# Optimization experiments

Hardware: AMD Instinct MI355X
Metric: run time of the kernel (lower is better)

## Reference

```python
import jax, jax.numpy as jnp
import numpy as np

T, B, E, H = 128, 1024, 1024, 1024  # batch must equal hidden (original code uses Whh @ h)


def setup_inputs() -> dict:
    key = jax.random.key(0)
    ks = jax.random.split(key, 10)
    s = 1.0 / np.sqrt(H).astype(np.float32)  # ~xavier scale, avoids gate saturation
    inp = {
        'X': jax.random.normal(ks[0], (T, B, E), dtype=jnp.float32),
        'Wii': jax.random.normal(ks[1], (E, H), dtype=jnp.float32) * s,
        'Whi': jax.random.normal(ks[2], (H, H), dtype=jnp.float32) * s,
        'bi': jnp.zeros((H,), dtype=jnp.float32),
        'Wif': jax.random.normal(ks[3], (E, H), dtype=jnp.float32) * s,
        'Whf': jax.random.normal(ks[4], (H, H), dtype=jnp.float32) * s,
        'bf': jnp.zeros((H,), dtype=jnp.float32),
        'Wig': jax.random.normal(ks[5], (E, H), dtype=jnp.float32) * s,
        'Whg': jax.random.normal(ks[6], (H, H), dtype=jnp.float32) * s,
        'bg': jnp.zeros((H,), dtype=jnp.float32),
        'Wio': jax.random.normal(ks[7], (E, H), dtype=jnp.float32) * s,
        'Who': jax.random.normal(ks[8], (H, H), dtype=jnp.float32) * s,
        'bo': jnp.zeros((H,), dtype=jnp.float32),
    }
    return inp


def reference(X, Wii, Whi, bi, Wif, Whf, bf, Wig, Whg, bg, Wio, Who, bo):
    # Faithful to the original: recurrent term is Whh @ h (NOT h @ Whh),
    # which requires batch == hidden as in the source module.
    batch = X.shape[1]
    hid = Wii.shape[1]
    h0 = jnp.zeros((batch, hid), dtype=X.dtype)
    c0 = jnp.zeros((batch, hid), dtype=X.dtype)

    def step(carry, x_t):
        h, c = carry
        i = jax.nn.sigmoid(x_t @ Wii + Whi @ h + bi)
        f = jax.nn.sigmoid(x_t @ Wif + Whf @ h + bf)
        g = jnp.tanh(x_t @ Wig + Whg @ h + bg)
        o = jax.nn.sigmoid(x_t @ Wio + Who @ h + bo)
        c_new = f * c + i * g
        h_new = o * jnp.tanh(c_new)
        return (h_new, c_new), h_new

    (h_t, c_t), hidden_sequence = jax.lax.scan(step, (h0, c0), X)
    return hidden_sequence, (h_t, c_t)
```

## Files before the change

kernel.cpp:

```cpp
#include <hip/hip_runtime.h>
#include <cstdint>

typedef __attribute__((ext_vector_type(8))) short bf16x8;
typedef __attribute__((ext_vector_type(4))) float f32x4;

#define AS1 __attribute__((address_space(1)))
#define AS3 __attribute__((address_space(3)))

__device__ __forceinline__ unsigned short f2bf(float f) {
  unsigned int u = __builtin_bit_cast(unsigned int, f);
  return (unsigned short)((u + 0x7fffu + ((u >> 16) & 1u)) >> 16);
}
__device__ __forceinline__ float bf2f(unsigned short h) {
  unsigned int u = ((unsigned int)h) << 16;
  return __builtin_bit_cast(float, u);
}
__device__ __forceinline__ float sigm(float x) { return 1.f / (1.f + __expf(-x)); }
__device__ __forceinline__ float tanh_f(float x) {
  float e = __expf(2.f * x);
  return 1.f - 2.f / (e + 1.f);
}
__device__ __forceinline__ void gload16(const void* g, void* l) {
  __builtin_amdgcn_global_load_lds((const AS1 unsigned int*)g, (AS3 unsigned int*)l, 16, 0, 0);
}
__device__ __forceinline__ int swz(int e) { return e ^ (((e >> 6) & 7) << 3); }


__global__ __launch_bounds__(256) void conv_wh_kernel(
    const float4* __restrict__ w0, const float4* __restrict__ w1,
    const float4* __restrict__ w2, const float4* __restrict__ w3,
    unsigned long long* __restrict__ dst) {
  int i = blockIdx.x * 256 + threadIdx.x;
  int g = i >> 18;
  const float4* s = g == 0 ? w0 : g == 1 ? w1 : g == 2 ? w2 : w3;
  float4 v = s[i & 0x3FFFF];
  unsigned long long p = (unsigned long long)f2bf(v.x) |
                         ((unsigned long long)f2bf(v.y) << 16) |
                         ((unsigned long long)f2bf(v.z) << 32) |
                         ((unsigned long long)f2bf(v.w) << 48);
  dst[i] = p;
}

__global__ __launch_bounds__(256) void conv_wiT_kernel(
    const float* __restrict__ w0, const float* __restrict__ w1,
    const float* __restrict__ w2, const float* __restrict__ w3,
    unsigned short* __restrict__ dst) {
  __shared__ unsigned short ls[64][72];
  int bid = blockIdx.x;
  int g = bid >> 8;
  int t2 = bid & 255;
  int tj = t2 & 15, tk = t2 >> 4;
  const float* W = g == 0 ? w0 : g == 1 ? w1 : g == 2 ? w2 : w3;
  int k0 = tk * 64, j0 = tj * 64;
  int ty = threadIdx.x >> 6, tx = threadIdx.x & 63;
#pragma unroll
  for (int r = 0; r < 16; ++r) {
    int k = k0 + ty * 16 + r;
    ls[tx][ty * 16 + r] = f2bf(W[k * 1024 + j0 + tx]);
  }
  __syncthreads();
#pragma unroll
  for (int r = 0; r < 16; ++r) {
    int jl = ty * 16 + r;
    dst[(size_t)(g * 1024 + j0 + jl) * 1024 + k0 + tx] = ls[jl][tx];
  }
}

__global__ __launch_bounds__(256) void conv_bias_kernel(
    const float* __restrict__ b0, const float* __restrict__ b1,
    const float* __restrict__ b2, const float* __restrict__ b3,
    float* __restrict__ dst) {
  int i = blockIdx.x * 256 + threadIdx.x;
  const float* s = (i >> 10) == 0 ? b0 : (i >> 10) == 1 ? b1 : (i >> 10) == 2 ? b2 : b3;
  dst[i] = s[i & 1023];
}

__global__ __launch_bounds__(256) void conv_x_kernel(
    const float4* __restrict__ src, unsigned long long* __restrict__ dst, int n4) {
  int i = blockIdx.x * 256 + threadIdx.x;
  if (i < n4) {
    float4 v = src[i];
    dst[i] = (unsigned long long)f2bf(v.x) |
             ((unsigned long long)f2bf(v.y) << 16) |
             ((unsigned long long)f2bf(v.z) << 32) |
             ((unsigned long long)f2bf(v.w) << 48);
  }
}

__global__ __launch_bounds__(256, 3) void xproj_gemm_kernel(
    const unsigned short* __restrict__ A,
    const unsigned short* __restrict__ Bt,
    unsigned short* __restrict__ C,
    int Mc) {
  __shared__ __align__(16) char smem[34816];
  unsigned short* lsA = (unsigned short*)smem;
  unsigned short* lsB = lsA + 8192;
  int xcd = blockIdx.x & 7;
  int i5 = blockIdx.x >> 3;
  int bn = xcd * 4 + (i5 & 3);
  int bm = i5 >> 2;
  int m0 = bm * 128, n0 = bn * 128;
  int tid = threadIdx.x, w = tid >> 6, lane = tid & 63;
  int wm = w >> 1, wn = w & 1;
  int l15 = lane & 15, l4 = lane >> 4;

  f32x4 acc[4][4];
#pragma unroll
  for (int i = 0; i < 4; ++i)
#pragma unroll
    for (int j = 0; j < 4; ++j) acc[i][j] = (f32x4)0.f;

  for (int ks = 0; ks < 16; ++ks) {
    int kk = ks * 64;
    __syncthreads();
#pragma unroll
    for (int ld = 0; ld < 4; ++ld) {
      int cid = ld * 256 + tid;
      int r = cid >> 3, kc = (cid & 7) * 8;
      int sk = kk + (kc ^ ((r & 7) << 3));
      gload16(&A[(size_t)(m0 + r) * 1024 + sk], &lsA[(ld * 256 + w * 64) * 8]);
      gload16(&Bt[(size_t)(n0 + r) * 1024 + sk], &lsB[(ld * 256 + w * 64) * 8]);
    }
    __syncthreads();
    bf16x8 af[4][2], bfr[4][2];
#pragma unroll
    for (int cm = 0; cm < 4; ++cm)
#pragma unroll
      for (int kss = 0; kss < 2; ++kss) {
        int e = (wm * 64 + cm * 16 + l15) * 64 + kss * 32 + l4 * 8;
        af[cm][kss] = *(const bf16x8*)&lsA[swz(e)];
      }
#pragma unroll
    for (int cn = 0; cn < 4; ++cn)
#pragma unroll
      for (int kss = 0; kss < 2; ++kss) {
        int e = (wn * 64 + cn * 16 + l15) * 64 + kss * 32 + l4 * 8;
        bfr[cn][kss] = *(const bf16x8*)&lsB[swz(e)];
      }
    __builtin_amdgcn_s_setprio(1);
#pragma unroll
    for (int cm = 0; cm < 4; ++cm)
#pragma unroll
      for (int cn = 0; cn < 4; ++cn)
#pragma unroll
        for (int kss = 0; kss < 2; ++kss)
          acc[cm][cn] = __builtin_amdgcn_mfma_f32_16x16x32_bf16(
              af[cm][kss], bfr[cn][kss], acc[cm][cn], 0, 0, 0);
    __builtin_amdgcn_s_setprio(0);
  }

  __syncthreads();
  unsigned short* lsC = (unsigned short*)smem;
#pragma unroll
  for (int cm = 0; cm < 4; ++cm)
#pragma unroll
    for (int cn = 0; cn < 4; ++cn)
#pragma unroll
      for (int r = 0; r < 4; ++r) {
        int row = wm * 64 + cm * 16 + l4 * 4 + r;
        int col = wn * 64 + cn * 16 + l15;
        lsC[row * 136 + col] = f2bf(acc[cm][cn][r]);
      }
  __syncthreads();
#pragma unroll
  for (int u = 0; u < 8; ++u) {
    int chunk = u * 256 + tid;
    int row = chunk >> 4, c8 = chunk & 15;
    bf16x8 v = *(const bf16x8*)&lsC[row * 136 + c8 * 8];
    *(bf16x8*)&C[(size_t)(m0 + row) * 4096 + n0 + c8 * 8] = v;
  }
}

__global__ __launch_bounds__(256) void lstm_step_kernel(
    const unsigned short* __restrict__ Wh,
    const unsigned short* __restrict__ hT,
    const unsigned short* __restrict__ Xp,
    const float* __restrict__ bias,
    float* __restrict__ cst,
    float* __restrict__ out_h,
    float* __restrict__ out_ht,
    float* __restrict__ out_ct,
    unsigned short* __restrict__ hT_next,
    int isLast) {
  __shared__ unsigned short lsA[3][128 * 64];
  __shared__ unsigned short lsB[3][64 * 64];
  int bx = blockIdx.x;
  int xcd = bx & 7, idx = bx >> 3;
  int bb = xcd * 4 + (idx & 3);
  int bj = idx >> 2;
  int b0 = bb * 32, j0 = bj * 64;
  int tid = threadIdx.x, w = tid >> 6, lane = tid & 63;
  int wm = w >> 1, wn = w & 1;
  int l15 = lane & 15, l4 = lane >> 4;
  int bbase = b0 + wm * 16 + l4 * 4;

  float bias_pre[4][2];
  float c_pre[2][4];
  unsigned short xp_pre[4][2][4];
#pragma unroll
  for (int n = 0; n < 2; ++n) {
    int j = j0 + wn * 32 + n * 16 + l15;
#pragma unroll
    for (int g = 0; g < 4; ++g) bias_pre[g][n] = bias[g * 1024 + j];
#pragma unroll
    for (int r = 0; r < 4; ++r) {
      c_pre[n][r] = cst[(size_t)(bbase + r) * 1024 + j];
#pragma unroll
      for (int g = 0; g < 4; ++g)
        xp_pre[g][n][r] = Xp[(size_t)(bbase + r) * 4096 + g * 1024 + j];
    }
  }

  f32x4 acc[4][2];
#pragma unroll
  for (int g = 0; g < 4; ++g)
#pragma unroll
    for (int n = 0; n < 2; ++n) acc[g][n] = (f32x4)0.f;

  auto stage = [&](int buf, int kk) {
#pragma unroll
    for (int ld = 0; ld < 4; ++ld) {
      int cid = ld * 256 + tid;
      int r = cid >> 3, kc = (cid & 7) * 8;
      int sk = kk + (kc ^ ((r & 7) << 3));
      int grow = ((r >> 4) & 3) * 1024 + b0 + (r >> 6) * 16 + (r & 15);
      gload16(&Wh[(size_t)grow * 1024 + sk], &lsA[buf][(ld * 256 + w * 64) * 8]);
    }
#pragma unroll
    for (int u = 0; u < 2; ++u) {
      int cid = u * 256 + tid;
      int r = cid >> 3, kc = (cid & 7) * 8;
      int sk = kk + (kc ^ ((r & 7) << 3));
      gload16(&hT[(size_t)(j0 + r) * 1024 + sk], &lsB[buf][(u * 256 + w * 64) * 8]);
    }
  };
  auto compute = [&](int buf) {
    bf16x8 af[4][2], bfr[2][2];
#pragma unroll
    for (int g = 0; g < 4; ++g)
#pragma unroll
      for (int kss = 0; kss < 2; ++kss) {
        int e = (wm * 64 + g * 16 + l15) * 64 + kss * 32 + l4 * 8;
        af[g][kss] = *(const bf16x8*)&lsA[buf][swz(e)];
      }
#pragma unroll
    for (int n = 0; n < 2; ++n)
#pragma unroll
      for (int kss = 0; kss < 2; ++kss) {
        int e = (wn * 32 + n * 16 + l15) * 64 + kss * 32 + l4 * 8;
        bfr[n][kss] = *(const bf16x8*)&lsB[buf][swz(e)];
      }
    __builtin_amdgcn_s_setprio(1);
#pragma unroll
    for (int g = 0; g < 4; ++g)
#pragma unroll
      for (int n = 0; n < 2; ++n)
#pragma unroll
        for (int kss = 0; kss < 2; ++kss)
          acc[g][n] = __builtin_amdgcn_mfma_f32_16x16x32_bf16(
              af[g][kss], bfr[n][kss], acc[g][n], 0, 0, 0);
    __builtin_amdgcn_s_setprio(0);
  };

  stage(0, 0);
  stage(1, 64);
#pragma unroll
  for (int it = 0; it < 16; ++it) {
    if (it < 15) asm volatile("s_waitcnt vmcnt(6)" ::: "memory");
    else         asm volatile("s_waitcnt vmcnt(0)" ::: "memory");
    __builtin_amdgcn_sched_barrier(0);
    __builtin_amdgcn_s_barrier();
    __builtin_amdgcn_sched_barrier(0);
    if (it + 2 < 16) stage((it + 2) % 3, (it + 2) * 64);
    compute(it % 3);
    asm volatile("s_waitcnt lgkmcnt(0)" ::: "memory");
    __builtin_amdgcn_sched_barrier(0);
  }

#pragma unroll
  for (int n = 0; n < 2; ++n) {
    int j = j0 + wn * 32 + n * 16 + l15;
    float hn[4], cn[4];
#pragma unroll
    for (int r = 0; r < 4; ++r) {
      int b = bbase + r;
      float pi = acc[0][n][r] + bf2f(xp_pre[0][n][r]) + bias_pre[0][n];
      float pf = acc[1][n][r] + bf2f(xp_pre[1][n][r]) + bias_pre[1][n];
      float pg = acc[2][n][r] + bf2f(xp_pre[2][n][r]) + bias_pre[2][n];
      float po = acc[3][n][r] + bf2f(xp_pre[3][n][r]) + bias_pre[3][n];
      float ig = sigm(pi), fg = sigm(pf), gg = tanh_f(pg), og = sigm(po);
      float c_new = fg * c_pre[n][r] + ig * gg;
      cst[(size_t)b * 1024 + j] = c_new;
      cn[r] = c_new;
      hn[r] = og * tanh_f(c_new);
      out_h[(size_t)b * 1024 + j] = hn[r];
    }
    unsigned long long hp = (unsigned long long)f2bf(hn[0]) |
                            ((unsigned long long)f2bf(hn[1]) << 16) |
                            ((unsigned long long)f2bf(hn[2]) << 32) |
                            ((unsigned long long)f2bf(hn[3]) << 48);
    *(unsigned long long*)&hT_next[(size_t)j * 1024 + bbase] = hp;
    if (isLast) {
#pragma unroll
      for (int r = 0; r < 4; ++r) {
        int b = bbase + r;
        out_ht[(size_t)b * 1024 + j] = hn[r];
        out_ct[(size_t)b * 1024 + j] = cn[r];
      }
    }
  }
}

extern "C" void kernel_launch(void* const* d_in, const int* in_sizes, int n_in,
                              void* d_out, int out_size, void* d_ws, size_t ws_size,
                              hipStream_t stream) {
  const float* X   = (const float*)d_in[0];
  const float* Wii = (const float*)d_in[1];
  const float* Whi = (const float*)d_in[2];
  const float* bi  = (const float*)d_in[3];
  const float* Wif = (const float*)d_in[4];
  const float* Whf = (const float*)d_in[5];
  const float* bfv = (const float*)d_in[6];
  const float* Wig = (const float*)d_in[7];
  const float* Whg = (const float*)d_in[8];
  const float* bg  = (const float*)d_in[9];
  const float* Wio = (const float*)d_in[10];
  const float* Who = (const float*)d_in[11];
  const float* bo  = (const float*)d_in[12];
  float* out = (float*)d_out;

  char* wsp = (char*)d_ws;
  size_t off = 0;
  auto walloc = [&](size_t b) -> void* {
    void* p = wsp + off;
    off += (b + 255) & ~(size_t)255;
    return p;
  };
  unsigned short* WiT = (unsigned short*)walloc(4096ull * 1024 * 2);
  unsigned short* Wh  = (unsigned short*)walloc(4096ull * 1024 * 2);
  float* bias = (float*)walloc(4096 * 4);
  unsigned short* hT0 = (unsigned short*)walloc(1024ull * 1024 * 2);
  unsigned short* hT1 = (unsigned short*)walloc(1024ull * 1024 * 2);
  float* cbuf = (float*)walloc(1024ull * 1024 * 4);
  size_t fixed = off;

  long long avail = (long long)ws_size - (long long)fixed - (1ll << 20);
  int Tc = (int)(avail / (10ll << 20));
  if (Tc < 1) Tc = 1;
  if (Tc > 128) Tc = 128;
  unsigned short* Xbf = (unsigned short*)walloc((size_t)Tc * 1024 * 1024 * 2);
  unsigned short* Xp  = (unsigned short*)walloc((size_t)Tc * 1024 * 4096 * 2);

  conv_wh_kernel<<<4096, 256, 0, stream>>>((const float4*)Whi, (const float4*)Whf,
                                           (const float4*)Whg, (const float4*)Who,
                                           (unsigned long long*)Wh);
  conv_wiT_kernel<<<1024, 256, 0, stream>>>(Wii, Wif, Wig, Wio, WiT);
  conv_bias_kernel<<<16, 256, 0, stream>>>(bi, bfv, bg, bo, bias);
  hipMemsetAsync(hT0, 0, 1024ull * 1024 * 2, stream);
  hipMemsetAsync(cbuf, 0, 1024ull * 1024 * 4, stream);

  for (int t0 = 0; t0 < 128; t0 += Tc) {
    int tc = (128 - t0 < Tc) ? (128 - t0) : Tc;
    int n4 = tc * 262144;
    conv_x_kernel<<<n4 / 256, 256, 0, stream>>>(
        (const float4*)(X + (size_t)t0 * 1048576),
        (unsigned long long*)Xbf, n4);
    xproj_gemm_kernel<<<tc * 256, 256, 0, stream>>>(Xbf, WiT, Xp, tc * 1024);
    for (int i = 0; i < tc; ++i) {
      int t = t0 + i;
      lstm_step_kernel<<<512, 256, 0, stream>>>(
          Wh, (t & 1) ? hT1 : hT0,
          Xp + (size_t)i * 1024 * 4096,
          bias, cbuf,
          out + (size_t)t * 1048576,
          out + 134217728ull,
          out + 135266304ull,
          (t & 1) ? hT0 : hT1,
          (t == 127) ? 1 : 0);
    }
  }
}
```

Before: 3.597 ms.

## Rewrite input-projection GEMM with 256x256 tiles and triple-buffered LDS pipeline

```diff
diff --git a/kernel.cpp b/kernel.cpp
--- a/kernel.cpp
+++ b/kernel.cpp
@@ -87,87 +87,100 @@
   }
 }
 
-__global__ __launch_bounds__(256, 3) void xproj_gemm_kernel(
+__global__ __launch_bounds__(512, 2) void xproj_gemm_kernel(
     const unsigned short* __restrict__ A,
     const unsigned short* __restrict__ Bt,
     unsigned short* __restrict__ C,
     int Mc) {
-  __shared__ __align__(16) char smem[34816];
-  unsigned short* lsA = (unsigned short*)smem;
-  unsigned short* lsB = lsA + 8192;
+  __shared__ __align__(16) unsigned short smem[3][2][256 * 32];
   int xcd = blockIdx.x & 7;
   int i5 = blockIdx.x >> 3;
-  int bn = xcd * 4 + (i5 & 3);
-  int bm = i5 >> 2;
-  int m0 = bm * 128, n0 = bn * 128;
+  int bn = xcd * 2 + (i5 & 1);
+  int bm = i5 >> 1;
+  int m0 = bm * 256, n0 = bn * 256;
   int tid = threadIdx.x, w = tid >> 6, lane = tid & 63;
-  int wm = w >> 1, wn = w & 1;
+  int wm = w >> 2, wn = w & 3;
   int l15 = lane & 15, l4 = lane >> 4;
 
-  f32x4 acc[4][4];
-#pragma unroll
-  for (int i = 0; i < 4; ++i)
+  f32x4 acc[8][4];
+#pragma unroll
+  for (int i = 0; i < 8; ++i)
 #pragma unroll
     for (int j = 0; j < 4; ++j) acc[i][j] = (f32x4)0.f;
 
-  for (int ks = 0; ks < 16; ++ks) {
-    int kk = ks * 64;
+  auto stage = [&](int buf, int kk) {
+#pragma unroll
+    for (int u = 0; u < 2; ++u) {
+      int cid = u * 512 + tid;
+      int r = cid >> 2, kc = (cid & 3) * 8;
+      gload16(&A[(size_t)(m0 + r) * 1024 + kk + kc],
+              &smem[buf][0][(u * 512 + w * 64) * 8]);
+    }
+#pragma unroll
+    for (int u = 0; u < 2; ++u) {
+      int cid = u * 512 + tid;
+      int r = cid >> 2, kc = (cid & 3) * 8;
+      gload16(&Bt[(size_t)(n0 + r) * 1024 + kk + kc],
+              &smem[buf][1][(u * 512 + w * 64) * 8]);
+    }
+  };
+  auto compute = [&](int buf) {
+    bf16x8 af[8], bfr[4];
+#pragma unroll
+    for (int mf = 0; mf < 8; ++mf)
+      af[mf] = *(const bf16x8*)&smem[buf][0][(wm * 128 + mf * 16 + l15) * 32 + l4 * 8];
+#pragma unroll
+    for (int nf = 0; nf < 4; ++nf)
+      bfr[nf] = *(const bf16x8*)&smem[buf][1][(wn * 64 + nf * 16 + l15) * 32 + l4 * 8];
+    __builtin_amdgcn_s_setprio(1);
+#pragma unroll
+    for (int mf = 0; mf < 8; ++mf)
+#pragma unroll
+      for (int nf = 0; nf < 4; ++nf)
+        acc[mf][nf] = __builtin_amdgcn_mfma_f32_16x16x32_bf16(
+            af[mf], bfr[nf], acc[mf][nf], 0, 0, 0);
+    __builtin_amdgcn_s_setprio(0);
+  };
+
+  stage(0, 0);
+  stage(1, 32);
+#pragma unroll
+  for (int it = 0; it < 32; ++it) {
+    if (it < 31) asm volatile("s_waitcnt vmcnt(4)" ::: "memory");
+    else         asm volatile("s_waitcnt vmcnt(0)" ::: "memory");
+    __builtin_amdgcn_sched_barrier(0);
+    __builtin_amdgcn_s_barrier();
+    __builtin_amdgcn_sched_barrier(0);
+    if (it + 2 < 32) stage((it + 2) % 3, (it + 2) * 32);
+    compute(it % 3);
+    asm volatile("s_waitcnt lgkmcnt(0)" ::: "memory");
+    __builtin_amdgcn_sched_barrier(0);
+  }
+
+  unsigned short* lsC = &smem[0][0][0];
+#pragma unroll
+  for (int h = 0; h < 2; ++h) {
     __syncthreads();
-#pragma unroll
-    for (int ld = 0; ld < 4; ++ld) {
-      int cid = ld * 256 + tid;
-      int r = cid >> 3, kc = (cid & 7) * 8;
-      int sk = kk + (kc ^ ((r & 7) << 3));
-      gload16(&A[(size_t)(m0 + r) * 1024 + sk], &lsA[(ld * 256 + w * 64) * 8]);
-      gload16(&Bt[(size_t)(n0 + r) * 1024 + sk], &lsB[(ld * 256 + w * 64) * 8]);
+    if ((wn >> 1) == h) {
+#pragma unroll
+      for (int mf = 0; mf < 8; ++mf)
+#pragma unroll
+        for (int nf = 0; nf < 4; ++nf)
+#pragma unroll
+          for (int r = 0; r < 4; ++r) {
+            int row = wm * 128 + mf * 16 + l4 * 4 + r;
+            int col = (wn & 1) * 64 + nf * 16 + l15;
+            lsC[row * 136 + col] = f2bf(acc[mf][nf][r]);
+          }
     }
     __syncthreads();
-    bf16x8 af[4][2], bfr[4][2];
-#pragma unroll
-    for (int cm = 0; cm < 4; ++cm)
-#pragma unroll
-      for (int kss = 0; kss < 2; ++kss) {
-        int e = (wm * 64 + cm * 16 + l15) * 64 + kss * 32 + l4 * 8;
-        af[cm][kss] = *(const bf16x8*)&lsA[swz(e)];
-      }
-#pragma unroll
-    for (int cn = 0; cn < 4; ++cn)
-#pragma unroll
-      for (int kss = 0; kss < 2; ++kss) {
-        int e = (wn * 64 + cn * 16 + l15) * 64 + kss * 32 + l4 * 8;
-        bfr[cn][kss] = *(const bf16x8*)&lsB[swz(e)];
-      }
-    __builtin_amdgcn_s_setprio(1);
-#pragma unroll
-    for (int cm = 0; cm < 4; ++cm)
-#pragma unroll
-      for (int cn = 0; cn < 4; ++cn)
-#pragma unroll
-        for (int kss = 0; kss < 2; ++kss)
-          acc[cm][cn] = __builtin_amdgcn_mfma_f32_16x16x32_bf16(
-              af[cm][kss], bfr[cn][kss], acc[cm][cn], 0, 0, 0);
-    __builtin_amdgcn_s_setprio(0);
-  }
-
-  __syncthreads();
-  unsigned short* lsC = (unsigned short*)smem;
-#pragma unroll
-  for (int cm = 0; cm < 4; ++cm)
-#pragma unroll
-    for (int cn = 0; cn < 4; ++cn)
-#pragma unroll
-      for (int r = 0; r < 4; ++r) {
-        int row = wm * 64 + cm * 16 + l4 * 4 + r;
-        int col = wn * 64 + cn * 16 + l15;
-        lsC[row * 136 + col] = f2bf(acc[cm][cn][r]);
-      }
-  __syncthreads();
-#pragma unroll
-  for (int u = 0; u < 8; ++u) {
-    int chunk = u * 256 + tid;
-    int row = chunk >> 4, c8 = chunk & 15;
-    bf16x8 v = *(const bf16x8*)&lsC[row * 136 + c8 * 8];
-    *(bf16x8*)&C[(size_t)(m0 + row) * 4096 + n0 + c8 * 8] = v;
+#pragma unroll
+    for (int u = 0; u < 8; ++u) {
+      int chunk = u * 512 + tid;
+      int row = chunk >> 4, c8 = chunk & 15;
+      bf16x8 v = *(const bf16x8*)&lsC[row * 136 + c8 * 8];
+      *(bf16x8*)&C[(size_t)(m0 + row) * 4096 + n0 + h * 128 + c8 * 8] = v;
+    }
   }
 }
 
@@ -365,7 +378,7 @@
     conv_x_kernel<<<n4 / 256, 256, 0, stream>>>(
         (const float4*)(X + (size_t)t0 * 1048576),
         (unsigned long long*)Xbf, n4);
-    xproj_gemm_kernel<<<tc * 256, 256, 0, stream>>>(Xbf, WiT, Xp, tc * 1024);
+    xproj_gemm_kernel<<<tc * 64, 512, 0, stream>>>(Xbf, WiT, Xp, tc * 1024);
     for (int i = 0; i < tc; ++i) {
       int t = t0 + i;
       lstm_step_kernel<<<512, 256, 0, stream>>>(
```

Result: no change. 3.599 ms (+0.0%).

## Overlap next chunk's input projection GEMM with recurrent step kernels

Applied to the files above, without the earlier changes.

```diff
diff --git a/kernel.cpp b/kernel.cpp
--- a/kernel.cpp
+++ b/kernel.cpp
@@ -3,6 +3,7 @@
 
 typedef __attribute__((ext_vector_type(8))) short bf16x8;
 typedef __attribute__((ext_vector_type(4))) float f32x4;
+typedef __attribute__((ext_vector_type(4))) unsigned int u32x4;
 
 #define AS1 __attribute__((address_space(1)))
 #define AS3 __attribute__((address_space(3)))
@@ -87,226 +88,223 @@
   }
 }
 
-__global__ __launch_bounds__(256, 3) void xproj_gemm_kernel(
-    const unsigned short* __restrict__ A,
-    const unsigned short* __restrict__ Bt,
-    unsigned short* __restrict__ C,
-    int Mc) {
-  __shared__ __align__(16) char smem[34816];
-  unsigned short* lsA = (unsigned short*)smem;
-  unsigned short* lsB = lsA + 8192;
-  int xcd = blockIdx.x & 7;
-  int i5 = blockIdx.x >> 3;
-  int bn = xcd * 4 + (i5 & 3);
-  int bm = i5 >> 2;
-  int m0 = bm * 128, n0 = bn * 128;
-  int tid = threadIdx.x, w = tid >> 6, lane = tid & 63;
-  int wm = w >> 1, wn = w & 1;
-  int l15 = lane & 15, l4 = lane >> 4;
-
-  f32x4 acc[4][4];
-#pragma unroll
-  for (int i = 0; i < 4; ++i)
-#pragma unroll
-    for (int j = 0; j < 4; ++j) acc[i][j] = (f32x4)0.f;
-
-  for (int ks = 0; ks < 16; ++ks) {
-    int kk = ks * 64;
-    __syncthreads();
-#pragma unroll
-    for (int ld = 0; ld < 4; ++ld) {
-      int cid = ld * 256 + tid;
-      int r = cid >> 3, kc = (cid & 7) * 8;
-      int sk = kk + (kc ^ ((r & 7) << 3));
-      gload16(&A[(size_t)(m0 + r) * 1024 + sk], &lsA[(ld * 256 + w * 64) * 8]);
-      gload16(&Bt[(size_t)(n0 + r) * 1024 + sk], &lsB[(ld * 256 + w * 64) * 8]);
-    }
-    __syncthreads();
-    bf16x8 af[4][2], bfr[4][2];
-#pragma unroll
-    for (int cm = 0; cm < 4; ++cm)
-#pragma unroll
-      for (int kss = 0; kss < 2; ++kss) {
-        int e = (wm * 64 + cm * 16 + l15) * 64 + kss * 32 + l4 * 8;
-        af[cm][kss] = *(const bf16x8*)&lsA[swz(e)];
-      }
-#pragma unroll
-    for (int cn = 0; cn < 4; ++cn)
-#pragma unroll
-      for (int kss = 0; kss < 2; ++kss) {
-        int e = (wn * 64 + cn * 16 + l15) * 64 + kss * 32 + l4 * 8;
-        bfr[cn][kss] = *(const bf16x8*)&lsB[swz(e)];
-      }
-    __builtin_amdgcn_s_setprio(1);
-#pragma unroll
-    for (int cm = 0; cm < 4; ++cm)
-#pragma unroll
-      for (int cn = 0; cn < 4; ++cn)
-#pragma unroll
-        for (int kss = 0; kss < 2; ++kss)
-          acc[cm][cn] = __builtin_amdgcn_mfma_f32_16x16x32_bf16(
-              af[cm][kss], bfr[cn][kss], acc[cm][cn], 0, 0, 0);
-    __builtin_amdgcn_s_setprio(0);
-  }
-
-  __syncthreads();
-  unsigned short* lsC = (unsigned short*)smem;
-#pragma unroll
-  for (int cm = 0; cm < 4; ++cm)
-#pragma unroll
-    for (int cn = 0; cn < 4; ++cn)
-#pragma unroll
-      for (int r = 0; r < 4; ++r) {
-        int row = wm * 64 + cm * 16 + l4 * 4 + r;
-        int col = wn * 64 + cn * 16 + l15;
-        lsC[row * 136 + col] = f2bf(acc[cm][cn][r]);
-      }
-  __syncthreads();
-#pragma unroll
-  for (int u = 0; u < 8; ++u) {
-    int chunk = u * 256 + tid;
-    int row = chunk >> 4, c8 = chunk & 15;
-    bf16x8 v = *(const bf16x8*)&lsC[row * 136 + c8 * 8];
-    *(bf16x8*)&C[(size_t)(m0 + row) * 4096 + n0 + c8 * 8] = v;
-  }
-}
-
-__global__ __launch_bounds__(256) void lstm_step_kernel(
+__global__ __launch_bounds__(256, 3) void fused_step_kernel(
     const unsigned short* __restrict__ Wh,
     const unsigned short* __restrict__ hT,
     const unsigned short* __restrict__ Xp,
     const float* __restrict__ bias,
     float* __restrict__ cst,
-    float* __restrict__ out_h,
-    float* __restrict__ out_ht,
+    float* __restrict__ out_h, float* __restrict__ out_ht,
     float* __restrict__ out_ct,
     unsigned short* __restrict__ hT_next,
-    int isLast) {
-  __shared__ unsigned short lsA[3][128 * 64];
-  __shared__ unsigned short lsB[3][64 * 64];
+    int isLast, int nStep,
+    const unsigned short* __restrict__ Axp,
+    const unsigned short* __restrict__ Bt,
+    unsigned short* __restrict__ Cxp,
+    int xTileBase) {
+  __shared__ __align__(16) char smem[49152];
+  int tid = threadIdx.x, w = tid >> 6, lane = tid & 63;
+  int l15 = lane & 15, l4 = lane >> 4;
   int bx = blockIdx.x;
-  int xcd = bx & 7, idx = bx >> 3;
-  int bb = xcd * 4 + (idx & 3);
-  int bj = idx >> 2;
-  int b0 = bb * 32, j0 = bj * 64;
-  int tid = threadIdx.x, w = tid >> 6, lane = tid & 63;
-  int wm = w >> 1, wn = w & 1;
-  int l15 = lane & 15, l4 = lane >> 4;
-  int bbase = b0 + wm * 16 + l4 * 4;
-
-  float bias_pre[4][2];
-  float c_pre[2][4];
-  unsigned short xp_pre[4][2][4];
-#pragma unroll
-  for (int n = 0; n < 2; ++n) {
-    int j = j0 + wn * 32 + n * 16 + l15;
-#pragma unroll
-    for (int g = 0; g < 4; ++g) bias_pre[g][n] = bias[g * 1024 + j];
-#pragma unroll
-    for (int r = 0; r < 4; ++r) {
-      c_pre[n][r] = cst[(size_t)(bbase + r) * 1024 + j];
+
+  if (bx < nStep) {
+    unsigned short* lsA0 = (unsigned short*)smem;
+    unsigned short* lsB0 = lsA0 + 16384;
+    int xcd = bx & 7, idx = bx >> 3;
+    int bb = xcd * 4 + (idx & 3);
+    int bj = idx >> 2;
+    int b0 = bb * 32, j0 = bj * 64;
+    int wm = w >> 1, wn = w & 1;
+    int bbase = b0 + wm * 16 + l4 * 4;
+
+    float bias_pre[4][2];
+    float c_pre[2][4];
+    unsigned short xp_pre[4][2][4];
+#pragma unroll
+    for (int n = 0; n < 2; ++n) {
+      int j = j0 + wn * 32 + n * 16 + l15;
+#pragma unroll
+      for (int g = 0; g < 4; ++g) bias_pre[g][n] = bias[g * 1024 + j];
+#pragma unroll
+      for (int r = 0; r < 4; ++r) {
+        c_pre[n][r] = cst[(size_t)(bbase + r) * 1024 + j];
+#pragma unroll
+        for (int g = 0; g < 4; ++g)
+          xp_pre[g][n][r] = Xp[(size_t)(bbase + r) * 4096 + g * 1024 + j];
+      }
+    }
+
+    f32x4 acc[4][2];
+#pragma unroll
+    for (int g = 0; g < 4; ++g)
+#pragma unroll
+      for (int n = 0; n < 2; ++n) acc[g][n] = (f32x4)0.f;
+
+    auto stage = [&](int buf, int kk) {
+      unsigned short* dA = lsA0 + buf * 8192;
+      unsigned short* dB = lsB0 + buf * 4096;
+#pragma unroll
+      for (int ld = 0; ld < 4; ++ld) {
+        int cid = ld * 256 + tid;
+        int r = cid >> 3, kc = (cid & 7) * 8;
+        int sk = kk + (kc ^ ((r & 7) << 3));
+        int grow = ((r >> 4) & 3) * 1024 + b0 + (r >> 6) * 16 + (r & 15);
+        gload16(&Wh[(size_t)grow * 1024 + sk], &dA[(ld * 256 + w * 64) * 8]);
+      }
+#pragma unroll
+      for (int u = 0; u < 2; ++u) {
+        int cid = u * 256 + tid;
+        int r = cid >> 3, kc = (cid & 7) * 8;
+        int sk = kk + (kc ^ ((r & 7) << 3));
+        gload16(&hT[(size_t)(j0 + r) * 1024 + sk], &dB[(u * 256 + w * 64) * 8]);
+      }
+    };
+    auto compute = [&](int buf) {
+      unsigned short* sA = lsA0 + buf * 8192;
+      unsigned short* sB = lsB0 + buf * 4096;
+      bf16x8 af[4][2], bfr[2][2];
 #pragma unroll
       for (int g = 0; g < 4; ++g)
-        xp_pre[g][n][r] = Xp[(size_t)(bbase + r) * 4096 + g * 1024 + j];
-    }
-  }
-
-  f32x4 acc[4][2];
-#pragma unroll
-  for (int g = 0; g < 4; ++g)
-#pragma unroll
-    for (int n = 0; n < 2; ++n) acc[g][n] = (f32x4)0.f;
-
-  auto stage = [&](int buf, int kk) {
-#pragma unroll
-    for (int ld = 0; ld < 4; ++ld) {
-      int cid = ld * 256 + tid;
-      int r = cid >> 3, kc = (cid & 7) * 8;
-      int sk = kk + (kc ^ ((r & 7) << 3));
-      int grow = ((r >> 4) & 3) * 1024 + b0 + (r >> 6) * 16 + (r & 15);
-      gload16(&Wh[(size_t)grow * 1024 + sk], &lsA[buf][(ld * 256 + w * 64) * 8]);
-    }
-#pragma unroll
-    for (int u = 0; u < 2; ++u) {
-      int cid = u * 256 + tid;
-      int r = cid >> 3, kc = (cid & 7) * 8;
-      int sk = kk + (kc ^ ((r & 7) << 3));
-      gload16(&hT[(size_t)(j0 + r) * 1024 + sk], &lsB[buf][(u * 256 + w * 64) * 8]);
-    }
-  };
-  auto compute = [&](int buf) {
-    bf16x8 af[4][2], bfr[2][2];
-#pragma unroll
-    for (int g = 0; g < 4; ++g)
-#pragma unroll
-      for (int kss = 0; kss < 2; ++kss) {
-        int e = (wm * 64 + g * 16 + l15) * 64 + kss * 32 + l4 * 8;
-        af[g][kss] = *(const bf16x8*)&lsA[buf][swz(e)];
-      }
-#pragma unroll
-    for (int n = 0; n < 2; ++n)
-#pragma unroll
-      for (int kss = 0; kss < 2; ++kss) {
-        int e = (wn * 32 + n * 16 + l15) * 64 + kss * 32 + l4 * 8;
-        bfr[n][kss] = *(const bf16x8*)&lsB[buf][swz(e)];
-      }
-    __builtin_amdgcn_s_setprio(1);
-#pragma unroll
-    for (int g = 0; g < 4; ++g)
+#pragma unroll
+        for (int kss = 0; kss < 2; ++kss) {
+          int e = (wm * 64 + g * 16 + l15) * 64 + kss * 32 + l4 * 8;
+          af[g][kss] = *(const bf16x8*)&sA[swz(e)];
+        }
 #pragma unroll
       for (int n = 0; n < 2; ++n)
 #pragma unroll
-        for (int kss = 0; kss < 2; ++kss)
-          acc[g][n] = __builtin_amdgcn_mfma_f32_16x16x32_bf16(
-              af[g][kss], bfr[n][kss], acc[g][n], 0, 0, 0);
-    __builtin_amdgcn_s_setprio(0);
-  };
-
-  stage(0, 0);
-  stage(1, 64);
-#pragma unroll
-  for (int it = 0; it < 16; ++it) {
-    if (it < 15) asm volatile("s_waitcnt vmcnt(6)" ::: "memory");
-    else         asm volatile("s_waitcnt vmcnt(0)" ::: "memory");
-    __builtin_amdgcn_sched_barrier(0);
-    __builtin_amdgcn_s_barrier();
-    __builtin_amdgcn_sched_barrier(0);
-    if (it + 2 < 16) stage((it + 2) % 3, (it + 2) * 64);
-    compute(it % 3);
-    asm volatile("s_waitcnt lgkmcnt(0)" ::: "memory");
-    __builtin_amdgcn_sched_barrier(0);
-  }
-
-#pragma unroll
-  for (int n = 0; n < 2; ++n) {
-    int j = j0 + wn * 32 + n * 16 + l15;
-    float hn[4], cn[4];
-#pragma unroll
-    for (int r = 0; r < 4; ++r) {
-      int b = bbase + r;
-      float pi = acc[0][n][r] + bf2f(xp_pre[0][n][r]) + bias_pre[0][n];
-      float pf = acc[1][n][r] + bf2f(xp_pre[1][n][r]) + bias_pre[1][n];
-      float pg = acc[2][n][r] + bf2f(xp_pre[2][n][r]) + bias_pre[2][n];
-      float po = acc[3][n][r] + bf2f(xp_pre[3][n][r]) + bias_pre[3][n];
-      float ig = sigm(pi), fg = sigm(pf), gg = tanh_f(pg), og = sigm(po);
-      float c_new = fg * c_pre[n][r] + ig * gg;
-      cst[(size_t)b * 1024 + j] = c_new;
-      cn[r] = c_new;
-      hn[r] = og * tanh_f(c_new);
-      out_h[(size_t)b * 1024 + j] = hn[r];
-    }
-    unsigned long long hp = (unsigned long long)f2bf(hn[0]) |
-                            ((unsigned long long)f2bf(hn[1]) << 16) |
-                            ((unsigned long long)f2bf(hn[2]) << 32) |
-                            ((unsigned long long)f2bf(hn[3]) << 48);
-    *(unsigned long long*)&hT_next[(size_t)j * 1024 + bbase] = hp;
-    if (isLast) {
+        for (int kss = 0; kss < 2; ++kss) {
+          int e = (wn * 32 + n * 16 + l15) * 64 + kss * 32 + l4 * 8;
+          bfr[n][kss] = *(const bf16x8*)&sB[swz(e)];
+        }
+      __builtin_amdgcn_s_setprio(1);
+#pragma unroll
+      for (int g = 0; g < 4; ++g)
+#pragma unroll
+        for (int n = 0; n < 2; ++n)
+#pragma unroll
+          for (int kss = 0; kss < 2; ++kss)
+            acc[g][n] = __builtin_amdgcn_mfma_f32_16x16x32_bf16(
+                af[g][kss], bfr[n][kss], acc[g][n], 0, 0, 0);
+      __builtin_amdgcn_s_setprio(0);
+    };
+
+    stage(0, 0);
+#pragma unroll
+    for (int it = 0; it < 16; ++it) {
+      asm volatile("s_waitcnt vmcnt(0)" ::: "memory");
+      __builtin_amdgcn_sched_barrier(0);
+      __builtin_amdgcn_s_barrier();
+      __builtin_amdgcn_sched_barrier(0);
+      if (it + 1 < 16) stage((it + 1) & 1, (it + 1) * 64);
+      compute(it & 1);
+      asm volatile("s_waitcnt lgkmcnt(0)" ::: "memory");
+      __builtin_amdgcn_sched_barrier(0);
+    }
+
+#pragma unroll
+    for (int n = 0; n < 2; ++n) {
+      int j = j0 + wn * 32 + n * 16 + l15;
+      float hn[4], cn[4];
 #pragma unroll
       for (int r = 0; r < 4; ++r) {
         int b = bbase + r;
-        out_ht[(size_t)b * 1024 + j] = hn[r];
-        out_ct[(size_t)b * 1024 + j] = cn[r];
-      }
+        float pi = acc[0][n][r] + bf2f(xp_pre[0][n][r]) + bias_pre[0][n];
+        float pf = acc[1][n][r] + bf2f(xp_pre[1][n][r]) + bias_pre[1][n];
+        float pg = acc[2][n][r] + bf2f(xp_pre[2][n][r]) + bias_pre[2][n];
+        float po = acc[3][n][r] + bf2f(xp_pre[3][n][r]) + bias_pre[3][n];
+        float ig = sigm(pi), fg = sigm(pf), gg = tanh_f(pg), og = sigm(po);
+        float c_new = fg * c_pre[n][r] + ig * gg;
+        cst[(size_t)b * 1024 + j] = c_new;
+        cn[r] = c_new;
+        hn[r] = og * tanh_f(c_new);
+        __builtin_nontemporal_store(hn[r], &out_h[(size_t)b * 1024 + j]);
+      }
+      unsigned long long hp = (unsigned long long)f2bf(hn[0]) |
+                              ((unsigned long long)f2bf(hn[1]) << 16) |
+                              ((unsigned long long)f2bf(hn[2]) << 32) |
+                              ((unsigned long long)f2bf(hn[3]) << 48);
+      *(unsigned long long*)&hT_next[(size_t)j * 1024 + bbase] = hp;
+      if (isLast) {
+#pragma unroll
+        for (int r = 0; r < 4; ++r) {
+          int b = bbase + r;
+          __builtin_nontemporal_store(hn[r], &out_ht[(size_t)b * 1024 + j]);
+          __builtin_nontemporal_store(cn[r], &out_ct[(size_t)b * 1024 + j]);
+        }
+      }
+    }
+  } else {
+    unsigned short* lsA = (unsigned short*)smem;
+    unsigned short* lsB = lsA + 8192;
+    int g = xTileBase + (bx - nStep);
+    int bm = g >> 5, bn = g & 31;
+    int m0 = bm * 128, n0 = bn * 128;
+    int wm = w >> 1, wn = w & 1;
+
+    f32x4 acc[4][4];
+#pragma unroll
+    for (int i = 0; i < 4; ++i)
+#pragma unroll
+      for (int j = 0; j < 4; ++j) acc[i][j] = (f32x4)0.f;
+
+    for (int ks = 0; ks < 16; ++ks) {
+      int kk = ks * 64;
+      __syncthreads();
+#pragma unroll
+      for (int ld = 0; ld < 4; ++ld) {
+        int cid = ld * 256 + tid;
+        int r = cid >> 3, kc = (cid & 7) * 8;
+        int sk = kk + (kc ^ ((r & 7) << 3));
+        gload16(&Axp[(size_t)(m0 + r) * 1024 + sk], &lsA[(ld * 256 + w * 64) * 8]);
+        gload16(&Bt[(size_t)(n0 + r) * 1024 + sk], &lsB[(ld * 256 + w * 64) * 8]);
+      }
+      __syncthreads();
+      bf16x8 af[4][2], bfr[4][2];
+#pragma unroll
+      for (int cm = 0; cm < 4; ++cm)
+#pragma unroll
+        for (int kss = 0; kss < 2; ++kss) {
+          int e = (wm * 64 + cm * 16 + l15) * 64 + kss * 32 + l4 * 8;
+          af[cm][kss] = *(const bf16x8*)&lsA[swz(e)];
+        }
+#pragma unroll
+      for (int cn = 0; cn < 4; ++cn)
+#pragma unroll
+        for (int kss = 0; kss < 2; ++kss) {
+          int e = (wn * 64 + cn * 16 + l15) * 64 + kss * 32 + l4 * 8;
+          bfr[cn][kss] = *(const bf16x8*)&lsB[swz(e)];
+        }
+#pragma unroll
+      for (int cm = 0; cm < 4; ++cm)
+#pragma unroll
+        for (int cn = 0; cn < 4; ++cn)
+#pragma unroll
+          for (int kss = 0; kss < 2; ++kss)
+            acc[cm][cn] = __builtin_amdgcn_mfma_f32_16x16x32_bf16(
+                af[cm][kss], bfr[cn][kss], acc[cm][cn], 0, 0, 0);
+    }
+
+    __syncthreads();
+    unsigned short* lsC = (unsigned short*)smem;
+#pragma unroll
+    for (int cm = 0; cm < 4; ++cm)
+#pragma unroll
+      for (int cn = 0; cn < 4; ++cn)
+#pragma unroll
+        for (int r = 0; r < 4; ++r) {
+          int row = wm * 64 + cm * 16 + l4 * 4 + r;
+          int col = wn * 64 + cn * 16 + l15;
+          lsC[row * 136 + col] = f2bf(acc[cm][cn][r]);
+        }
+    __syncthreads();
+#pragma unroll
+    for (int u = 0; u < 8; ++u) {
+      int chunk = u * 256 + tid;
+      int row = chunk >> 4, c8 = chunk & 15;
+      u32x4 v = *(const u32x4*)&lsC[row * 136 + c8 * 8];
+      __builtin_nontemporal_store(
+          v, (u32x4*)&Cxp[(size_t)(m0 + row) * 4096 + n0 + c8 * 8]);
     }
   }
 }
@@ -345,11 +343,14 @@
   size_t fixed = off;
 
   long long avail = (long long)ws_size - (long long)fixed - (1ll << 20);
-  int Tc = (int)(avail / (10ll << 20));
-  if (Tc < 1) Tc = 1;
-  if (Tc > 128) Tc = 128;
-  unsigned short* Xbf = (unsigned short*)walloc((size_t)Tc * 1024 * 1024 * 2);
-  unsigned short* Xp  = (unsigned short*)walloc((size_t)Tc * 1024 * 4096 * 2);
+  int Tc = 16;
+  while (Tc > 1 && (long long)Tc * 2 * (10ll << 20) > avail) Tc >>= 1;
+  int nc = 128 / Tc;
+  unsigned short* Xbf[2], *Xp[2];
+  Xbf[0] = (unsigned short*)walloc((size_t)Tc * 1024 * 1024 * 2);
+  Xbf[1] = (unsigned short*)walloc((size_t)Tc * 1024 * 1024 * 2);
+  Xp[0]  = (unsigned short*)walloc((size_t)Tc * 1024 * 4096 * 2);
+  Xp[1]  = (unsigned short*)walloc((size_t)Tc * 1024 * 4096 * 2);
 
   conv_wh_kernel<<<4096, 256, 0, stream>>>((const float4*)Whi, (const float4*)Whf,
                                            (const float4*)Whg, (const float4*)Who,
@@ -359,24 +360,31 @@
   hipMemsetAsync(hT0, 0, 1024ull * 1024 * 2, stream);
   hipMemsetAsync(cbuf, 0, 1024ull * 1024 * 4, stream);
 
-  for (int t0 = 0; t0 < 128; t0 += Tc) {
-    int tc = (128 - t0 < Tc) ? (128 - t0) : Tc;
-    int n4 = tc * 262144;
-    conv_x_kernel<<<n4 / 256, 256, 0, stream>>>(
-        (const float4*)(X + (size_t)t0 * 1048576),
-        (unsigned long long*)Xbf, n4);
-    xproj_gemm_kernel<<<tc * 256, 256, 0, stream>>>(Xbf, WiT, Xp, tc * 1024);
-    for (int i = 0; i < tc; ++i) {
-      int t = t0 + i;
-      lstm_step_kernel<<<512, 256, 0, stream>>>(
+  conv_x_kernel<<<Tc * 1024, 256, 0, stream>>>(
+      (const float4*)X, (unsigned long long*)Xbf[0], Tc * 262144);
+  fused_step_kernel<<<Tc * 256, 256, 0, stream>>>(
+      Wh, hT0, Xp[0], bias, cbuf, out, out, out, hT1, 0,
+      0 , Xbf[0], WiT, Xp[0], 0);
+
+  for (int i = 0; i < nc; ++i) {
+    int cur = i & 1, nxt = cur ^ 1;
+    if (i + 1 < nc)
+      conv_x_kernel<<<Tc * 1024, 256, 0, stream>>>(
+          (const float4*)(X + (size_t)(i + 1) * Tc * 1048576),
+          (unsigned long long*)Xbf[nxt], Tc * 262144);
+    for (int s = 0; s < Tc; ++s) {
+      int t = i * Tc + s;
+      int nX = (i + 1 < nc) ? 256 : 0;
+      fused_step_kernel<<<512 + nX, 256, 0, stream>>>(
           Wh, (t & 1) ? hT1 : hT0,
-          Xp + (size_t)i * 1024 * 4096,
+          Xp[cur] + (size_t)s * 4194304,
           bias, cbuf,
           out + (size_t)t * 1048576,
           out + 134217728ull,
           out + 135266304ull,
           (t & 1) ? hT0 : hT1,
-          (t == 127) ? 1 : 0);
-    }
-  }
-}
+          (t == 127) ? 1 : 0,
+          512 , Xbf[nxt], WiT, Xp[nxt], s * 256);
+    }
+  }
+}
```

Result: slower. 3.769 ms (+4.8%).
